# Kernel optimization log

Hardware: AMD Instinct MI355X
Metric: run time of the kernel (lower is better)

## Reference

```python
import jax, jax.numpy as jnp
import numpy as np
from jax import lax

B, C, T, H, W = 1, 64, 16, 48, 48
RC = C // 16

def conv2d(x, w, b=None, stride=1, pad=1):
    out = lax.conv_general_dilated(x, w, (stride, stride), [(pad, pad), (pad, pad)],
                                   dimension_numbers=('NCHW', 'OIHW', 'NCHW'))
    return out if b is None else out + b[None, :, None, None]

def dwconv3d(x, w, b, pad, dil):
    out = lax.conv_general_dilated(x, w, (1, 1, 1), [(p, p) for p in pad], rhs_dilation=dil,
                                   dimension_numbers=('NCDHW', 'OIDHW', 'NCDHW'),
                                   feature_group_count=x.shape[1])
    return out + b[None, :, None, None, None]

def grid_sample_zeros(img, grid):
    # img [N,Cc,Hh,Ww], grid [N,Hg,Wg,2] with (x,y) in [-1,1]; bilinear, zeros padding, align_corners=False
    N, Cc, Hh, Ww = img.shape
    gx, gy = grid[..., 0], grid[..., 1]
    x = ((gx + 1.0) * Ww - 1.0) * 0.5
    y = ((gy + 1.0) * Hh - 1.0) * 0.5
    x0 = jnp.floor(x); y0 = jnp.floor(y)
    imgf = img.reshape(N, Cc, Hh * Ww)
    def corner(xi, yi, wgt):
        valid = (xi >= 0) & (xi < Ww) & (yi >= 0) & (yi < Hh)
        idx = (jnp.clip(yi, 0, Hh - 1) * Ww + jnp.clip(xi, 0, Ww - 1)).astype(jnp.int32)
        vals = jnp.take_along_axis(imgf, idx.reshape(N, 1, -1), axis=2).reshape(N, Cc, *xi.shape[1:])
        return vals * (wgt * valid)[:, None]
    return (corner(x0, y0, (x0 + 1 - x) * (y0 + 1 - y)) + corner(x0 + 1, y0, (x - x0) * (y0 + 1 - y))
            + corner(x0, y0 + 1, (x0 + 1 - x) * (y - y0)) + corner(x0 + 1, y0 + 1, (x - x0) * (y - y0)))

def corr_attn(a, w1, w2):
    avg = jnp.mean(a, axis=1, keepdims=True)
    mx = jnp.max(a, axis=1, keepdims=True)
    var = jnp.var(a, axis=1, keepdims=True, ddof=1)  # torch unbiased var
    y = jax.nn.sigmoid(conv2d(jnp.concatenate([avg, mx], axis=1), w1, pad=1) + conv2d(var, w2, pad=1))
    return a * y

def setup_inputs() -> dict:
    key = jax.random.key(0)
    ks = jax.random.split(key, 16)
    def n(k, shape, s=0.05):
        return jax.random.normal(k, shape, jnp.float32) * s
    return {
        'x': jax.random.normal(ks[0], (B, C, T, H, W), jnp.float32),
        'w_dc2': n(ks[1], (C, C)),
        'w_ofs_l': n(ks[2], (2, C, 3, 3)), 'b_ofs_l': n(ks[3], (2,)),
        'w_ofs_r': n(ks[4], (2, C, 3, 3)), 'b_ofs_r': n(ks[5], (2,)),
        'ca_w1': n(ks[6], (1, 2, 3, 3)), 'ca_w2': n(ks[7], (1, 1, 3, 3)),
        'w_down': n(ks[8], (RC, C)),
        'sa1_w': n(ks[9], (RC, 1, 9, 3, 3)), 'sa1_b': n(ks[10], (RC,)),
        'sa2_w': n(ks[11], (RC, 1, 9, 3, 3)), 'sa2_b': n(ks[12], (RC,)),
        'sa3_w': n(ks[13], (RC, 1, 9, 3, 3)), 'sa3_b': n(ks[14], (RC,)),
        'weights': jnp.ones(3, jnp.float32) / 3,
        'weights2': jnp.ones(2, jnp.float32) / 2,
        'w_back': n(ks[15], (C, RC)),
    }

def reference(x, w_dc2, w_ofs_l, b_ofs_l, w_ofs_r, b_ofs_r, ca_w1, ca_w2, w_down,
              sa1_w, sa1_b, sa2_w, sa2_b, sa3_w, sa3_b, weights, weights2, w_back):
    Bq, Cq, Tq, Hq, Wq = x.shape
    x2 = jnp.einsum('oc,bcthw->bothw', w_dc2, x)  # 1x1x1 conv3d
    left_move = jnp.concatenate([x2[:, :, 1:], x2[:, :, -1:]], axis=2)
    right_move = jnp.concatenate([x2[:, :, :1], x2[:, :, :-1]], axis=2)
    to2d = lambda t: t.transpose(0, 2, 1, 3, 4).reshape(Bq * Tq, Cq, Hq, Wq)
    off_l = conv2d(to2d(x + left_move), w_ofs_l, b_ofs_l, stride=2, pad=1)  # [BT,2,H2,W2]
    off_r = conv2d(to2d(x + right_move), w_ofs_r, b_ofs_r, stride=2, pad=1)
    H2, W2 = off_l.shape[-2:]
    gx, gy = jnp.meshgrid(jnp.arange(W2, dtype=x.dtype), jnp.arange(H2, dtype=x.dtype), indexing='xy')
    base = jnp.stack([gx, gy]) * 2.0  # [2,H2,W2]; matches create_grid_like * 2
    def norm_grid(v):  # faithful to normalize_grid (ch0 scaled by H2-1, ch1 by W2-1)
        gh = 2.0 * v[:, 0] / max(H2 - 1, 1) - 1.0
        gw = 2.0 * v[:, 1] / max(W2 - 1, 1) - 1.0
        return jnp.stack([gh, gw], axis=-1)
    left_part = grid_sample_zeros(to2d(left_move), norm_grid(base[None] + off_l))
    right_part = grid_sample_zeros(to2d(right_move), norm_grid(base[None] + off_r))
    to5d = lambda t: t.reshape(Bq, Tq, Cq, H2, W2).transpose(0, 2, 1, 3, 4)  # [B,C,T,H2,W2]
    left_part = to5d(left_part); right_part = to5d(right_part)
    def branch(part, wscale):
        aff = jnp.einsum('bcthw,bctsd->bthwsd', x, part)  # all-pairs correlation volume
        a = aff.reshape(Bq * Tq, Hq, Wq, H2 * W2).transpose(0, 3, 1, 2)
        a = corr_attn(a, ca_w1, ca_w2)
        a = a.reshape(Bq, Tq, H2, W2, Hq, Wq).transpose(0, 1, 4, 5, 2, 3)  # [B,T,H,W,H2,W2]
        return jnp.einsum('bctsd,bthwsd->bcthw', part, jax.nn.sigmoid(a) - 0.5) * wscale
    features = branch(left_part, weights2[0]) + branch(right_part, weights2[1])
    xd = jnp.einsum('oc,bcthw->bothw', w_down, x)  # channel reduction
    agg = (dwconv3d(xd, sa1_w, sa1_b, (4, 1, 1), (1, 1, 1)) * weights[0]
           + dwconv3d(xd, sa2_w, sa2_b, (4, 2, 2), (1, 2, 2)) * weights[1]
           + dwconv3d(xd, sa3_w, sa3_b, (4, 3, 3), (1, 3, 3)) * weights[2])
    agg = jnp.einsum('oc,bcthw->bothw', w_back, agg)
    return features * (jax.nn.sigmoid(agg) - 0.5)
```

## Files before the change

kernel.cpp:

```cpp
#include <hip/hip_runtime.h>
#include <hip/hip_bf16.h>

#define T_    16
#define C_    64
#define H_    48
#define W_    48
#define HW_   2304
#define THW_  36864
#define CTHW_ 2359296
#define H2_   24
#define W2_   24
#define SD_   576
#define RC_   4
#define SDT_  72

typedef short short8 __attribute__((ext_vector_type(8)));
typedef short short4v __attribute__((ext_vector_type(4)));
typedef float f32x4 __attribute__((ext_vector_type(4)));

__device__ __forceinline__ float sigm(float v) { return 1.f / (1.f + __expf(-v)); }
__device__ __forceinline__ unsigned short f2bf(float v) {
    __hip_bfloat16 h = __float2bfloat16(v);
    union { __hip_bfloat16 h; unsigned short u; } cv; cv.h = h; return cv.u;
}
__device__ __forceinline__ float bf2f(unsigned short u) {
    return __uint_as_float((unsigned)u << 16);
}

__global__ __launch_bounds__(256) void k_pre(const float* __restrict__ x,
                                             const float* __restrict__ w,
                                             const float* __restrict__ w_down,
                                             float* __restrict__ x2T,
                                             unsigned short* __restrict__ xbh,
                                             unsigned short* __restrict__ xbl,
                                             float* __restrict__ xd) {
    int base = blockIdx.x * 64;
    __shared__ float wl[64 * 65];
    __shared__ float xt[4096];
    __shared__ float ld[64 * 65];
    __shared__ float wd[256];
    int tid = threadIdx.x;
    for (int i = tid; i < 4096; i += 256) wl[(i >> 6) * 65 + (i & 63)] = w[i];
    for (int i = tid; i < 4096; i += 256) {
        float v = x[(size_t)(i >> 6) * THW_ + base + (i & 63)];
        xt[i] = v;
        ld[(i >> 6) * 65 + (i & 63)] = v;
    }
    if (tid < 256) wd[tid] = w_down[tid];
    __syncthreads();
    {
        int o_grp = tid >> 4, u_grp = tid & 15;
        float acc[4][4] = {};
        const float4* xt4 = (const float4*)xt;
        for (int c = 0; c < 64; ++c) {
            float xa[4];
            *(float4*)xa = xt4[c * 16 + u_grp];
            #pragma unroll
            for (int i = 0; i < 4; ++i) {
                float wv = wl[(o_grp * 4 + i) * 65 + c];
                #pragma unroll
                for (int g = 0; g < 4; ++g) acc[i][g] += wv * xa[g];
            }
        }
        #pragma unroll
        for (int g = 0; g < 4; ++g) {
            float4 v = make_float4(acc[0][g], acc[1][g], acc[2][g], acc[3][g]);
            *(float4*)&x2T[(size_t)(base + u_grp * 4 + g) * 64 + o_grp * 4] = v;
        }
    }
    {
        int r = tid >> 6, u = tid & 63;
        float a = 0.f;
        #pragma unroll 8
        for (int c = 0; c < 64; ++c) a += wd[r * 64 + c] * xt[c * 64 + u];
        xd[(size_t)r * THW_ + base + u] = a;
    }
    for (int i = tid; i < 4096; i += 256) {
        int u = i >> 6, c = i & 63;
        float v = ld[c * 65 + u];
        unsigned short h = f2bf(v);
        xbh[(size_t)(base + u) * 64 + c] = h;
        xbl[(size_t)(base + u) * 64 + c] = f2bf(v - bf2f(h));
    }
}

__global__ __launch_bounds__(256) void k_off(const unsigned short* __restrict__ xbh,
                                             const unsigned short* __restrict__ xbl,
                                             const float* __restrict__ x2T,
                                             const float* __restrict__ w_l,
                                             const float* __restrict__ b_l,
                                             const float* __restrict__ w_r,
                                             const float* __restrict__ b_r,
                                             float* __restrict__ off) {
    __shared__ float wlds[2304];
    int tid = threadIdx.x;
    for (int i = tid; i < 2304; i += 256) wlds[i] = (i < 1152) ? w_l[i] : w_r[i - 1152];
    __syncthreads();
    int wg = blockIdx.x * 4 + (tid >> 6);
    int lane = tid & 63;
    int j = wg % 24, i = (wg / 24) % 24, t = (wg / 576) % 16, side = wg / 9216;
    int ts = (side == 0) ? min(t + 1, T_ - 1) : max(t - 1, 0);
    const float* wp = wlds + side * 1152;
    const unsigned short* xhb = xbh + ((size_t)t * HW_) * 64 + lane;
    const unsigned short* xlb = xbl + ((size_t)t * HW_) * 64 + lane;
    const float* x2l = x2T + (size_t)ts * HW_ * 64 + lane;
    float a0 = 0.f, a1 = 0.f;
    for (int ki = 0; ki < 3; ++ki) {
        int hh = 2 * i - 1 + ki;
        if (hh < 0 || hh >= H_) continue;
        for (int kj = 0; kj < 3; ++kj) {
            int ww = 2 * j - 1 + kj;
            if (ww < 0 || ww >= W_) continue;
            int pos = hh * W_ + ww;
            float s = bf2f(xhb[(size_t)pos * 64]) + bf2f(xlb[(size_t)pos * 64])
                    + x2l[(size_t)pos * 64];
            int tap = ki * 3 + kj;
            a0 += s * wp[lane * 9 + tap];
            a1 += s * wp[576 + lane * 9 + tap];
        }
    }
    #pragma unroll
    for (int m = 32; m >= 1; m >>= 1) {
        a0 += __shfl_xor(a0, m);
        a1 += __shfl_xor(a1, m);
    }
    if (lane == 0) {
        const float* bb = (side == 0) ? b_l : b_r;
        int ob = (side * 16 + t) * 1152 + i * 24 + j;
        off[ob] = a0 + bb[0];
        off[ob + 576] = a1 + bb[1];
    }
}

__global__ __launch_bounds__(256) void k_gs(const float* __restrict__ x2T,
                                            const float* __restrict__ off,
                                            unsigned short* __restrict__ pch,
                                            unsigned short* __restrict__ pcl) {
    int wg = blockIdx.x * 4 + (threadIdx.x >> 6);
    int lane = threadIdx.x & 63;
    int sd = wg % 576;
    int t = (wg / 576) % 16;
    int side = wg / 9216;
    int d = sd % W2_, s = sd / W2_;
    const float* offp = off + (side * 16 + t) * 1152;
    float v0 = 2.f * (float)d + offp[sd];
    float v1 = 2.f * (float)s + offp[576 + sd];
    float xf = 48.f * v0 / 23.f - 0.5f;
    float yf = 48.f * v1 / 23.f - 0.5f;
    float x0 = floorf(xf), y0 = floorf(yf);
    int ix0 = (int)x0, iy0 = (int)y0;
    float fx = xf - x0, fy = yf - y0;
    float w00 = (1.f - fx) * (1.f - fy), w10 = fx * (1.f - fy);
    float w01 = (1.f - fx) * fy,         w11 = fx * fy;
    bool vx0 = (ix0 >= 0 && ix0 < W_), vx1 = (ix0 + 1 >= 0 && ix0 + 1 < W_);
    bool vy0 = (iy0 >= 0 && iy0 < H_), vy1 = (iy0 + 1 >= 0 && iy0 + 1 < H_);
    int cx0 = min(max(ix0, 0), W_ - 1), cx1 = min(max(ix0 + 1, 0), W_ - 1);
    int cy0 = min(max(iy0, 0), H_ - 1), cy1 = min(max(iy0 + 1, 0), H_ - 1);
    float m00 = (vx0 && vy0) ? w00 : 0.f;
    float m10 = (vx1 && vy0) ? w10 : 0.f;
    float m01 = (vx0 && vy1) ? w01 : 0.f;
    float m11 = (vx1 && vy1) ? w11 : 0.f;
    int ts = (side == 0) ? min(t + 1, T_ - 1) : max(t - 1, 0);
    const float* img = x2T + (size_t)ts * HW_ * 64;
    float val = m00 * img[(size_t)(cy0 * W_ + cx0) * 64 + lane]
              + m10 * img[(size_t)(cy0 * W_ + cx1) * 64 + lane]
              + m01 * img[(size_t)(cy1 * W_ + cx0) * 64 + lane]
              + m11 * img[(size_t)(cy1 * W_ + cx1) * 64 + lane];
    size_t idx = ((size_t)(side * 16 + t) * 576 + sd) * 64 + lane;
    unsigned short h = f2bf(val);
    pch[idx] = h;
    pcl[idx] = f2bf(val - bf2f(h));
}

__global__ __launch_bounds__(256) void k_stats(const unsigned short* __restrict__ xbh,
                                               const unsigned short* __restrict__ xbl,
                                               const unsigned short* __restrict__ pch,
                                               const unsigned short* __restrict__ pcl,
                                               float* __restrict__ stats) {
    int bid = blockIdx.x;
    int side = bid & 1;
    int tb = bid >> 1;
    int t = tb / 36, hwt = tb % 36;
    int base = t * HW_ + hwt * 64;
    __shared__ __attribute__((aligned(16))) unsigned short psh[64 * SDT_];
    __shared__ __attribute__((aligned(16))) unsigned short psl[64 * SDT_];
    int tid = threadIdx.x;
    int lane = tid & 63, wv = tid >> 6;
    int quad = lane >> 4, l15 = lane & 15;
    int m0 = wv * 16;
    const unsigned short* xrh = xbh + (size_t)(base + m0 + l15) * 64;
    const unsigned short* xrl = xbl + (size_t)(base + m0 + l15) * 64;
    short8 ah0 = *(const short8*)&xrh[quad * 8];
    short8 ah1 = *(const short8*)&xrh[32 + quad * 8];
    short8 al0 = *(const short8*)&xrl[quad * 8];
    short8 al1 = *(const short8*)&xrl[32 + quad * 8];
    int sH[4], sC[4];
    #pragma unroll
    for (int k = 0; k < 4; ++k) { int i = tid + k * 256; sH[k] = i >> 4; sC[k] = i & 15; }
    const unsigned short* phb = pch + (size_t)(side * 16 + t) * 576 * 64;
    const unsigned short* plb = pcl + (size_t)(side * 16 + t) * 576 * 64;
    uint2 pf_h[4], pf_l[4];
    #pragma unroll
    for (int k = 0; k < 4; ++k) {
        pf_h[k] = *(const uint2*)&phb[(size_t)sH[k] * 64 + sC[k] * 4];
        pf_l[k] = *(const uint2*)&plb[(size_t)sH[k] * 64 + sC[k] * 4];
    }
    #pragma unroll
    for (int k = 0; k < 4; ++k) {
        *(uint2*)&psh[sH[k] * SDT_ + sC[k] * 4] = pf_h[k];
        *(uint2*)&psl[sH[k] * SDT_ + sC[k] * 4] = pf_l[k];
    }
    #pragma unroll
    for (int k = 0; k < 4; ++k) {
        pf_h[k] = *(const uint2*)&phb[4096 + (size_t)sH[k] * 64 + sC[k] * 4];
        pf_l[k] = *(const uint2*)&plb[4096 + (size_t)sH[k] * 64 + sC[k] * 4];
    }
    float sum[4] = {}, sq[4] = {};
    float mx[4] = {-1e30f, -1e30f, -1e30f, -1e30f};
    for (int kt = 0; kt < 9; ++kt) {
        __syncthreads();
        #pragma unroll
        for (int tile = 0; tile < 4; ++tile) {
            short8 bh0 = *(const short8*)&psh[(tile * 16 + l15) * SDT_ + quad * 8];
            short8 bh1 = *(const short8*)&psh[(tile * 16 + l15) * SDT_ + 32 + quad * 8];
            short8 bl0 = *(const short8*)&psl[(tile * 16 + l15) * SDT_ + quad * 8];
            short8 bl1 = *(const short8*)&psl[(tile * 16 + l15) * SDT_ + 32 + quad * 8];
            f32x4 dacc = {0.f, 0.f, 0.f, 0.f};
            dacc = __builtin_amdgcn_mfma_f32_16x16x32_bf16(ah0, bh0, dacc, 0, 0, 0);
            dacc = __builtin_amdgcn_mfma_f32_16x16x32_bf16(ah1, bh1, dacc, 0, 0, 0);
            dacc = __builtin_amdgcn_mfma_f32_16x16x32_bf16(ah0, bl0, dacc, 0, 0, 0);
            dacc = __builtin_amdgcn_mfma_f32_16x16x32_bf16(ah1, bl1, dacc, 0, 0, 0);
            dacc = __builtin_amdgcn_mfma_f32_16x16x32_bf16(al0, bh0, dacc, 0, 0, 0);
            dacc = __builtin_amdgcn_mfma_f32_16x16x32_bf16(al1, bh1, dacc, 0, 0, 0);
            #pragma unroll
            for (int r = 0; r < 4; ++r) {
                float v = dacc[r];
                sum[r] += v; sq[r] += v * v; mx[r] = fmaxf(mx[r], v);
            }
        }
        if (kt < 8) {
            __syncthreads();
            #pragma unroll
            for (int k = 0; k < 4; ++k) {
                *(uint2*)&psh[sH[k] * SDT_ + sC[k] * 4] = pf_h[k];
                *(uint2*)&psl[sH[k] * SDT_ + sC[k] * 4] = pf_l[k];
            }
            if (kt < 7) {
                const unsigned short* ph = phb + (size_t)(kt + 2) * 4096;
                const unsigned short* pl = plb + (size_t)(kt + 2) * 4096;
                #pragma unroll
                for (int k = 0; k < 4; ++k) {
                    pf_h[k] = *(const uint2*)&ph[(size_t)sH[k] * 64 + sC[k] * 4];
                    pf_l[k] = *(const uint2*)&pl[(size_t)sH[k] * 64 + sC[k] * 4];
                }
            }
        }
    }
    #pragma unroll
    for (int m = 1; m < 16; m <<= 1)
        #pragma unroll
        for (int r = 0; r < 4; ++r) {
            sum[r] += __shfl_xor(sum[r], m);
            sq[r]  += __shfl_xor(sq[r], m);
            mx[r]   = fmaxf(mx[r], __shfl_xor(mx[r], m));
        }
    if (l15 == 0) {
        #pragma unroll
        for (int r = 0; r < 4; ++r) {
            int thw = base + m0 + quad * 4 + r;
            stats[(side * 3 + 0) * THW_ + thw] = sum[r] * (1.f / 576.f);
            stats[(side * 3 + 1) * THW_ + thw] = mx[r];
            stats[(side * 3 + 2) * THW_ + thw] =
                (sq[r] - sum[r] * sum[r] * (1.f / 576.f)) * (1.f / 575.f);
        }
    }
}

__global__ __launch_bounds__(256) void k_aux(const float* __restrict__ stats,
                      const float* __restrict__ ca_w1,
                      const float* __restrict__ ca_w2, float* __restrict__ yb,
                      const float* __restrict__ xd,
                      const float* __restrict__ w1, const float* __restrict__ b1,
                      const float* __restrict__ w2, const float* __restrict__ b2,
                      const float* __restrict__ w3, const float* __restrict__ b3,
                      const float* __restrict__ wts, float* __restrict__ agg0,
                      const unsigned short* __restrict__ pch,
                      unsigned short* __restrict__ partb) {
    __shared__ unsigned short ld[64 * 68];
    int blk = blockIdx.x;
    int tid = threadIdx.x;
    if (blk < (2 * THW_) / 256) {
        int idx = blk * 256 + tid;
        int side = idx / THW_, thw = idx % THW_;
        int w = thw % W_, h = (thw / W_) % H_, t = thw / HW_;
        const float* avg = stats + (side * 3 + 0) * THW_ + t * HW_;
        const float* mxp = stats + (side * 3 + 1) * THW_ + t * HW_;
        const float* var = stats + (side * 3 + 2) * THW_ + t * HW_;
        float acc = 0.f;
        for (int ki = 0; ki < 3; ++ki) {
            int hh = h - 1 + ki;
            if (hh < 0 || hh >= H_) continue;
            for (int kj = 0; kj < 3; ++kj) {
                int ww = w - 1 + kj;
                if (ww < 0 || ww >= W_) continue;
                int p = hh * W_ + ww;
                int kk = ki * 3 + kj;
                acc += ca_w1[kk] * avg[p] + ca_w1[9 + kk] * mxp[p] + ca_w2[kk] * var[p];
            }
        }
        yb[idx] = sigm(acc);
    } else if (blk < (2 * THW_) / 256 + (RC_ * THW_) / 256) {
        int idx = (blk - (2 * THW_) / 256) * 256 + tid;
        int w = idx % W_;
        int h = (idx / W_) % H_;
        int t = (idx / HW_) % T_;
        int r = idx / THW_;
        const float* xr = xd + r * THW_;
        const float* wk_arr[3] = {w1, w2, w3};
        const float* bs_arr[3] = {b1, b2, b3};
        float tot = 0.f;
        for (int m = 0; m < 3; ++m) {
            int dil = m + 1;
            float acc = bs_arr[m][r];
            const float* wk = wk_arr[m] + r * 81;
            for (int kt = 0; kt < 9; ++kt) {
                int tt = t - 4 + kt;
                if (tt < 0 || tt >= T_) continue;
                for (int kh = 0; kh < 3; ++kh) {
                    int hh = h + (kh - 1) * dil;
                    if (hh < 0 || hh >= H_) continue;
                    for (int kw = 0; kw < 3; ++kw) {
                        int wwp = w + (kw - 1) * dil;
                        if (wwp < 0 || wwp >= W_) continue;
                        acc += xr[tt * HW_ + hh * W_ + wwp] * wk[kt * 9 + kh * 3 + kw];
                    }
                }
            }
            tot += acc * wts[m];
        }
        agg0[idx] = tot;
    } else {
        int b2 = blk - ((2 * THW_) / 256 + (RC_ * THW_) / 256);
        int st = b2 / 9;
        int sdt = b2 % 9;
        const unsigned short* src = pch + ((size_t)st * 576 + sdt * 64) * 64;
        for (int i = tid; i < 4096; i += 256) ld[(i >> 6) * 68 + (i & 63)] = src[i];
        __syncthreads();
        unsigned short* dst = partb + (size_t)st * 64 * 576 + sdt * 64;
        for (int i = tid; i < 4096; i += 256) {
            int c = i >> 6, sdl = i & 63;
            dst[(size_t)c * 576 + sdl] = ld[sdl * 68 + c];
        }
    }
}

__global__ __launch_bounds__(256) void k_final(const unsigned short* __restrict__ xbh,
                                               const unsigned short* __restrict__ xbl,
                                               const unsigned short* __restrict__ pch,
                                               const unsigned short* __restrict__ pcl,
                                               const unsigned short* __restrict__ partb,
                                               const float* __restrict__ yb,
                                               const float* __restrict__ weights2,
                                               const float* __restrict__ agg0,
                                               const float* __restrict__ w_back,
                                               float* __restrict__ out) {
    int bid = blockIdx.x;
    int side = bid & 1;
    int tb = bid >> 1;
    int t = tb / 36, hwt = tb % 36;
    int base = t * HW_ + hwt * 64;
    int st = side * 16 + t;
    __shared__ __attribute__((aligned(16))) unsigned short psh[64 * SDT_];
    __shared__ __attribute__((aligned(16))) unsigned short psl[64 * SDT_];
    __shared__ __attribute__((aligned(16))) unsigned short wt[64 * SDT_];
    int tid = threadIdx.x;
    int lane = tid & 63, wv = tid >> 6;
    int quad = lane >> 4, l15 = lane & 15;
    int m0 = wv * 16;
    const unsigned short* xrh = xbh + (size_t)(base + m0 + l15) * 64;
    const unsigned short* xrl = xbl + (size_t)(base + m0 + l15) * 64;
    short8 ah0 = *(const short8*)&xrh[quad * 8];
    short8 ah1 = *(const short8*)&xrh[32 + quad * 8];
    short8 al0 = *(const short8*)&xrl[quad * 8];
    short8 al1 = *(const short8*)&xrl[32 + quad * 8];
    float yvs = yb[(size_t)side * THW_ + base + m0 + l15];
    int sH[4], sC[4];
    #pragma unroll
    for (int k = 0; k < 4; ++k) { int i = tid + k * 256; sH[k] = i >> 4; sC[k] = i & 15; }
    const unsigned short* phb = pch + (size_t)st * 576 * 64;
    const unsigned short* plb = pcl + (size_t)st * 576 * 64;
    const unsigned short* pbb = partb + (size_t)st * 64 * 576 + (size_t)(m0 + l15) * 576;
    uint2 pf_h[4], pf_l[4];
    short8 pbn0, pbn1;
    #pragma unroll
    for (int k = 0; k < 4; ++k) {
        pf_h[k] = *(const uint2*)&phb[(size_t)sH[k] * 64 + sC[k] * 4];
        pf_l[k] = *(const uint2*)&plb[(size_t)sH[k] * 64 + sC[k] * 4];
    }
    pbn0 = *(const short8*)&pbb[quad * 8];
    pbn1 = *(const short8*)&pbb[32 + quad * 8];
    #pragma unroll
    for (int k = 0; k < 4; ++k) {
        *(uint2*)&psh[sH[k] * SDT_ + sC[k] * 4] = pf_h[k];
        *(uint2*)&psl[sH[k] * SDT_ + sC[k] * 4] = pf_l[k];
    }
    #pragma unroll
    for (int k = 0; k < 4; ++k) {
        pf_h[k] = *(const uint2*)&phb[4096 + (size_t)sH[k] * 64 + sC[k] * 4];
        pf_l[k] = *(const uint2*)&plb[4096 + (size_t)sH[k] * 64 + sC[k] * 4];
    }
    f32x4 acc[4] = {};
    for (int kt = 0; kt < 9; ++kt) {
        __syncthreads();
        #pragma unroll
        for (int tile = 0; tile < 4; ++tile) {
            short8 bh0 = *(const short8*)&psh[(tile * 16 + l15) * SDT_ + quad * 8];
            short8 bh1 = *(const short8*)&psh[(tile * 16 + l15) * SDT_ + 32 + quad * 8];
            short8 bl0 = *(const short8*)&psl[(tile * 16 + l15) * SDT_ + quad * 8];
            short8 bl1 = *(const short8*)&psl[(tile * 16 + l15) * SDT_ + 32 + quad * 8];
            f32x4 dacc = {0.f, 0.f, 0.f, 0.f};
            dacc = __builtin_amdgcn_mfma_f32_16x16x32_bf16(bh0, ah0, dacc, 0, 0, 0);
            dacc = __builtin_amdgcn_mfma_f32_16x16x32_bf16(bh1, ah1, dacc, 0, 0, 0);
            dacc = __builtin_amdgcn_mfma_f32_16x16x32_bf16(bl0, ah0, dacc, 0, 0, 0);
            dacc = __builtin_amdgcn_mfma_f32_16x16x32_bf16(bl1, ah1, dacc, 0, 0, 0);
            dacc = __builtin_amdgcn_mfma_f32_16x16x32_bf16(bh0, al0, dacc, 0, 0, 0);
            dacc = __builtin_amdgcn_mfma_f32_16x16x32_bf16(bh1, al1, dacc, 0, 0, 0);
            short4v wq;
            #pragma unroll
            for (int r = 0; r < 4; ++r)
                wq[r] = (short)f2bf(sigm(dacc[r] * yvs) - 0.5f);
            *(short4v*)&wt[(m0 + l15) * SDT_ + tile * 16 + quad * 4] = wq;
        }
        __syncthreads();
        short8 pA0 = pbn0, pA1 = pbn1;
        if (kt < 8) {
            #pragma unroll
            for (int k = 0; k < 4; ++k) {
                *(uint2*)&psh[sH[k] * SDT_ + sC[k] * 4] = pf_h[k];
                *(uint2*)&psl[sH[k] * SDT_ + sC[k] * 4] = pf_l[k];
            }
            if (kt < 7) {
                const unsigned short* ph = phb + (size_t)(kt + 2) * 4096;
                const unsigned short* pl = plb + (size_t)(kt + 2) * 4096;
                #pragma unroll
                for (int k = 0; k < 4; ++k) {
                    pf_h[k] = *(const uint2*)&ph[(size_t)sH[k] * 64 + sC[k] * 4];
                    pf_l[k] = *(const uint2*)&pl[(size_t)sH[k] * 64 + sC[k] * 4];
                }
            }
            const unsigned short* pbr = pbb + (kt + 1) * 64;
            pbn0 = *(const short8*)&pbr[quad * 8];
            pbn1 = *(const short8*)&pbr[32 + quad * 8];
        }
        #pragma unroll
        for (int tile = 0; tile < 4; ++tile) {
            short8 wb0 = *(const short8*)&wt[(tile * 16 + l15) * SDT_ + quad * 8];
            short8 wb1 = *(const short8*)&wt[(tile * 16 + l15) * SDT_ + 32 + quad * 8];
            acc[tile] = __builtin_amdgcn_mfma_f32_16x16x32_bf16(pA0, wb0, acc[tile], 0, 0, 0);
            acc[tile] = __builtin_amdgcn_mfma_f32_16x16x32_bf16(pA1, wb1, acc[tile], 0, 0, 0);
        }
    }
    float w2s = weights2[side];
    #pragma unroll
    for (int tile = 0; tile < 4; ++tile) {
        int thw = base + tile * 16 + l15;
        #pragma unroll
        for (int r = 0; r < 4; ++r) {
            int c = m0 + quad * 4 + r;
            float a = 0.f;
            #pragma unroll
            for (int rr = 0; rr < RC_; ++rr) a += w_back[c * RC_ + rr] * agg0[rr * THW_ + thw];
            atomicAdd(&out[(size_t)c * THW_ + thw],
                      acc[tile][r] * w2s * (sigm(a) - 0.5f));
        }
    }
}

extern "C" void kernel_launch(void* const* d_in, const int* in_sizes, int n_in,
                              void* d_out, int out_size, void* d_ws, size_t ws_size,
                              hipStream_t stream) {
    const float* x       = (const float*)d_in[0];
    const float* w_dc2   = (const float*)d_in[1];
    const float* w_ofs_l = (const float*)d_in[2];
    const float* b_ofs_l = (const float*)d_in[3];
    const float* w_ofs_r = (const float*)d_in[4];
    const float* b_ofs_r = (const float*)d_in[5];
    const float* ca_w1   = (const float*)d_in[6];
    const float* ca_w2   = (const float*)d_in[7];
    const float* w_down  = (const float*)d_in[8];
    const float* sa1_w   = (const float*)d_in[9];
    const float* sa1_b   = (const float*)d_in[10];
    const float* sa2_w   = (const float*)d_in[11];
    const float* sa2_b   = (const float*)d_in[12];
    const float* sa3_w   = (const float*)d_in[13];
    const float* sa3_b   = (const float*)d_in[14];
    const float* weights = (const float*)d_in[15];
    const float* weights2= (const float*)d_in[16];
    const float* w_back  = (const float*)d_in[17];
    float* out = (float*)d_out;

    float* ws    = (float*)d_ws;
    float* x2T   = ws;
    float* stats = x2T;
    float* yb    = stats + 2 * 3 * THW_;
    float* agg0  = yb + 2 * THW_;
    unsigned short* partb = (unsigned short*)(agg0 + RC_ * THW_);
    float* off   = ws + CTHW_;
    unsigned short* xbh = (unsigned short*)(off + 2 * T_ * 2 * SD_);
    unsigned short* xbl = xbh + CTHW_;
    unsigned short* pch = xbl + CTHW_;
    unsigned short* pcl = pch + 2 * 16 * 576 * 64;
    float* xd    = (float*)(pcl + 2 * 16 * 576 * 64);

    k_pre<<<THW_ / 64, 256, 0, stream>>>(x, w_dc2, w_down, x2T, xbh, xbl, xd);
    k_off<<<(2 * 16 * 576) / 4, 256, 0, stream>>>(xbh, xbl, x2T, w_ofs_l, b_ofs_l,
                                                  w_ofs_r, b_ofs_r, off);
    k_gs<<<(2 * 16 * 576) / 4, 256, 0, stream>>>(x2T, off, pch, pcl);
    k_stats<<<2 * 16 * 36, 256, 0, stream>>>(xbh, xbl, pch, pcl, stats);
    k_aux<<<(2 * THW_) / 256 + (RC_ * THW_) / 256 + 32 * 9, 256, 0, stream>>>(
        stats, ca_w1, ca_w2, yb, xd, sa1_w, sa1_b, sa2_w, sa2_b,
        sa3_w, sa3_b, weights, agg0, pch, partb);
    k_final<<<2 * 16 * 36, 256, 0, stream>>>(xbh, xbl, pch, pcl, partb, yb, weights2,
                                             agg0, w_back, out);
}
```

Measured before the change: 243.0 us.

## Keep attention weights in registers and double-buffer part tiles in k_final

Each wave's sigmoid-weighted correlation tile no longer goes through a shared-memory round trip. The tile stays in registers and feeds the second MFMA directly as the B operand; the accumulator layout is reorganised so each wave owns 16 spatial positions across all 64 channels. The part tiles in LDS are double-buffered, so only one barrier is needed per k-step instead of two. The A operand for the second GEMM is now read straight from global memory as short4 pieces each iteration, and the agg0 loads are hoisted per thread. This trades more global traffic and register pressure for fewer LDS writes and fewer syncs.

```diff
diff --git a/kernel.cpp b/kernel.cpp
--- a/kernel.cpp
+++ b/kernel.cpp
@@ -370,9 +370,8 @@
     int t = tb / 36, hwt = tb % 36;
     int base = t * HW_ + hwt * 64;
     int st = side * 16 + t;
-    __shared__ __attribute__((aligned(16))) unsigned short psh[64 * SDT_];
-    __shared__ __attribute__((aligned(16))) unsigned short psl[64 * SDT_];
-    __shared__ __attribute__((aligned(16))) unsigned short wt[64 * SDT_];
+    __shared__ __attribute__((aligned(16))) unsigned short pah[2][64 * SDT_];
+    __shared__ __attribute__((aligned(16))) unsigned short pal[2][64 * SDT_];
     int tid = threadIdx.x;
     int lane = tid & 63, wv = tid >> 6;
     int quad = lane >> 4, l15 = lane & 15;
@@ -389,35 +388,47 @@
     for (int k = 0; k < 4; ++k) { int i = tid + k * 256; sH[k] = i >> 4; sC[k] = i & 15; }
     const unsigned short* phb = pch + (size_t)st * 576 * 64;
     const unsigned short* plb = pcl + (size_t)st * 576 * 64;
-    const unsigned short* pbb = partb + (size_t)st * 64 * 576 + (size_t)(m0 + l15) * 576;
+    const unsigned short* pbs = partb + (size_t)st * 64 * 576;
     uint2 pf_h[4], pf_l[4];
-    short8 pbn0, pbn1;
     #pragma unroll
     for (int k = 0; k < 4; ++k) {
         pf_h[k] = *(const uint2*)&phb[(size_t)sH[k] * 64 + sC[k] * 4];
         pf_l[k] = *(const uint2*)&plb[(size_t)sH[k] * 64 + sC[k] * 4];
     }
-    pbn0 = *(const short8*)&pbb[quad * 8];
-    pbn1 = *(const short8*)&pbb[32 + quad * 8];
-    #pragma unroll
-    for (int k = 0; k < 4; ++k) {
-        *(uint2*)&psh[sH[k] * SDT_ + sC[k] * 4] = pf_h[k];
-        *(uint2*)&psl[sH[k] * SDT_ + sC[k] * 4] = pf_l[k];
-    }
-    #pragma unroll
-    for (int k = 0; k < 4; ++k) {
-        pf_h[k] = *(const uint2*)&phb[4096 + (size_t)sH[k] * 64 + sC[k] * 4];
-        pf_l[k] = *(const uint2*)&plb[4096 + (size_t)sH[k] * 64 + sC[k] * 4];
-    }
     f32x4 acc[4] = {};
     for (int kt = 0; kt < 9; ++kt) {
+        int b = kt & 1;
+        #pragma unroll
+        for (int k = 0; k < 4; ++k) {
+            *(uint2*)&pah[b][sH[k] * SDT_ + sC[k] * 4] = pf_h[k];
+            *(uint2*)&pal[b][sH[k] * SDT_ + sC[k] * 4] = pf_l[k];
+        }
+        if (kt < 8) {
+            const unsigned short* ph = phb + (size_t)(kt + 1) * 4096;
+            const unsigned short* pl = plb + (size_t)(kt + 1) * 4096;
+            #pragma unroll
+            for (int k = 0; k < 4; ++k) {
+                pf_h[k] = *(const uint2*)&ph[(size_t)sH[k] * 64 + sC[k] * 4];
+                pf_l[k] = *(const uint2*)&pl[(size_t)sH[k] * 64 + sC[k] * 4];
+            }
+        }
         __syncthreads();
+        short4v pa[4][4];
+        #pragma unroll
+        for (int ct = 0; ct < 4; ++ct) {
+            const unsigned short* pr = pbs + (size_t)(ct * 16 + l15) * 576 + kt * 64 + quad * 4;
+            pa[ct][0] = *(const short4v*)&pr[0];
+            pa[ct][1] = *(const short4v*)&pr[16];
+            pa[ct][2] = *(const short4v*)&pr[32];
+            pa[ct][3] = *(const short4v*)&pr[48];
+        }
+        short4v wt4[4];
         #pragma unroll
         for (int tile = 0; tile < 4; ++tile) {
-            short8 bh0 = *(const short8*)&psh[(tile * 16 + l15) * SDT_ + quad * 8];
-            short8 bh1 = *(const short8*)&psh[(tile * 16 + l15) * SDT_ + 32 + quad * 8];
-            short8 bl0 = *(const short8*)&psl[(tile * 16 + l15) * SDT_ + quad * 8];
-            short8 bl1 = *(const short8*)&psl[(tile * 16 + l15) * SDT_ + 32 + quad * 8];
+            short8 bh0 = *(const short8*)&pah[b][(tile * 16 + l15) * SDT_ + quad * 8];
+            short8 bh1 = *(const short8*)&pah[b][(tile * 16 + l15) * SDT_ + 32 + quad * 8];
+            short8 bl0 = *(const short8*)&pal[b][(tile * 16 + l15) * SDT_ + quad * 8];
+            short8 bl1 = *(const short8*)&pal[b][(tile * 16 + l15) * SDT_ + 32 + quad * 8];
             f32x4 dacc = {0.f, 0.f, 0.f, 0.f};
             dacc = __builtin_amdgcn_mfma_f32_16x16x32_bf16(bh0, ah0, dacc, 0, 0, 0);
             dacc = __builtin_amdgcn_mfma_f32_16x16x32_bf16(bh1, ah1, dacc, 0, 0, 0);
@@ -429,49 +440,33 @@
             #pragma unroll
             for (int r = 0; r < 4; ++r)
                 wq[r] = (short)f2bf(sigm(dacc[r] * yvs) - 0.5f);
-            *(short4v*)&wt[(m0 + l15) * SDT_ + tile * 16 + quad * 4] = wq;
-        }
-        __syncthreads();
-        short8 pA0 = pbn0, pA1 = pbn1;
-        if (kt < 8) {
-            #pragma unroll
-            for (int k = 0; k < 4; ++k) {
-                *(uint2*)&psh[sH[k] * SDT_ + sC[k] * 4] = pf_h[k];
-                *(uint2*)&psl[sH[k] * SDT_ + sC[k] * 4] = pf_l[k];
-            }
-            if (kt < 7) {
-                const unsigned short* ph = phb + (size_t)(kt + 2) * 4096;
-                const unsigned short* pl = plb + (size_t)(kt + 2) * 4096;
-                #pragma unroll
-                for (int k = 0; k < 4; ++k) {
-                    pf_h[k] = *(const uint2*)&ph[(size_t)sH[k] * 64 + sC[k] * 4];
-                    pf_l[k] = *(const uint2*)&pl[(size_t)sH[k] * 64 + sC[k] * 4];
-                }
-            }
-            const unsigned short* pbr = pbb + (kt + 1) * 64;
-            pbn0 = *(const short8*)&pbr[quad * 8];
-            pbn1 = *(const short8*)&pbr[32 + quad * 8];
-        }
-        #pragma unroll
-        for (int tile = 0; tile < 4; ++tile) {
-            short8 wb0 = *(const short8*)&wt[(tile * 16 + l15) * SDT_ + quad * 8];
-            short8 wb1 = *(const short8*)&wt[(tile * 16 + l15) * SDT_ + 32 + quad * 8];
-            acc[tile] = __builtin_amdgcn_mfma_f32_16x16x32_bf16(pA0, wb0, acc[tile], 0, 0, 0);
-            acc[tile] = __builtin_amdgcn_mfma_f32_16x16x32_bf16(pA1, wb1, acc[tile], 0, 0, 0);
+            wt4[tile] = wq;
+        }
+        short8 wf01 = __builtin_shufflevector(wt4[0], wt4[1], 0, 1, 2, 3, 4, 5, 6, 7);
+        short8 wf23 = __builtin_shufflevector(wt4[2], wt4[3], 0, 1, 2, 3, 4, 5, 6, 7);
+        #pragma unroll
+        for (int ct = 0; ct < 4; ++ct) {
+            short8 a01 = __builtin_shufflevector(pa[ct][0], pa[ct][1], 0, 1, 2, 3, 4, 5, 6, 7);
+            short8 a23 = __builtin_shufflevector(pa[ct][2], pa[ct][3], 0, 1, 2, 3, 4, 5, 6, 7);
+            acc[ct] = __builtin_amdgcn_mfma_f32_16x16x32_bf16(a01, wf01, acc[ct], 0, 0, 0);
+            acc[ct] = __builtin_amdgcn_mfma_f32_16x16x32_bf16(a23, wf23, acc[ct], 0, 0, 0);
         }
     }
     float w2s = weights2[side];
-    #pragma unroll
-    for (int tile = 0; tile < 4; ++tile) {
-        int thw = base + tile * 16 + l15;
+    int thw = base + m0 + l15;
+    float agv[RC_];
+    #pragma unroll
+    for (int rr = 0; rr < RC_; ++rr) agv[rr] = agg0[rr * THW_ + thw];
+    #pragma unroll
+    for (int ct = 0; ct < 4; ++ct) {
         #pragma unroll
         for (int r = 0; r < 4; ++r) {
-            int c = m0 + quad * 4 + r;
+            int c = ct * 16 + quad * 4 + r;
             float a = 0.f;
             #pragma unroll
-            for (int rr = 0; rr < RC_; ++rr) a += w_back[c * RC_ + rr] * agg0[rr * THW_ + thw];
+            for (int rr = 0; rr < RC_; ++rr) a += w_back[c * RC_ + rr] * agv[rr];
             atomicAdd(&out[(size_t)c * THW_ + thw],
-                      acc[tile][r] * w2s * (sigm(a) - 0.5f));
+                      acc[ct][r] * w2s * (sigm(a) - 0.5f));
         }
     }
 }
```

Measured after the change: 287.2 us. 1.18x slower.
